# Performance work log

Measured on AMD Instinct MI355X. Metric: run time of the kernel, lower is better.

## Reference

```python
import jax, jax.numpy as jnp
import numpy as np

DIM = 1024
HEADS = 8
DIM_HEAD = 64
DIM_INNER = HEADS * DIM_HEAD  # 512


def setup_inputs() -> dict:
    key = jax.random.key(0)
    k1, k2, k3, k4 = jax.random.split(key, 4)
    x = jax.random.normal(k1, (1, 4096, DIM), dtype=jnp.float32)
    gamma = jnp.ones((DIM,), dtype=jnp.float32)
    w_qkv = jax.random.normal(k2, (DIM, 3 * DIM_INNER), dtype=jnp.float32) * (DIM ** -0.5)
    w_out = jax.random.normal(k3, (DIM_INNER, DIM), dtype=jnp.float32) * (DIM_INNER ** -0.5)
    return {"x": x, "gamma": gamma, "w_qkv": w_qkv, "w_out": w_out}


def _rmsnorm(x, gamma):
    # F.normalize(x, dim=-1) * sqrt(dim) * gamma
    norm = jnp.sqrt(jnp.sum(x * x, axis=-1, keepdims=True))
    x = x / jnp.maximum(norm, 1e-12)
    return x * (DIM ** 0.5) * gamma


def reference(x, gamma, w_qkv, w_out):
    b, n, _ = x.shape
    h, d = HEADS, DIM_HEAD
    normed = _rmsnorm(x, gamma)
    qkv = normed @ w_qkv  # [b, n, 3*h*d]
    qkv = qkv.reshape(b, n, 3, h, d)
    q = jnp.transpose(qkv[:, :, 0], (0, 2, 1, 3))  # b h n d
    k = jnp.transpose(qkv[:, :, 1], (0, 2, 1, 3))
    v = jnp.transpose(qkv[:, :, 2], (0, 2, 1, 3))
    # default_attention (faithful: scales q by d**0.5 as in source)
    q = q * (d ** 0.5)
    sim = jnp.einsum('bhid,bhjd->bhij', q, k)
    mask_value = -jnp.finfo(sim.dtype).max
    causal_mask = jnp.triu(jnp.ones((n, n), dtype=bool), 1)
    sim = jnp.where(causal_mask, mask_value, sim)
    attn = jax.nn.softmax(sim, axis=-1)
    out = jnp.einsum('bhij,bhjd->bhid', attn, v)  # b h n d
    out = jnp.transpose(out, (0, 2, 1, 3)).reshape(b, n, h * d)
    return out @ w_out  # [b, n, dim]
```

## Files before the change

### kernel.cpp

```cpp
#include <hip/hip_runtime.h>
#include <math.h>

#define SEQ 4096
#define DIM 1024
#define HEADS 8
#define DINNER 512
#define QKVW 1536
#define PAD 80
#define NCHUNK 4
#define CHUNK_KT 16

typedef unsigned short u16;
typedef __attribute__((ext_vector_type(8))) short s8v;
typedef __attribute__((ext_vector_type(4))) float f4v;
#define MFMA(a, b, c) __builtin_amdgcn_mfma_f32_16x16x32_bf16(a, b, c, 0, 0, 0)

__device__ __forceinline__ u16 f2bf(float f) {
    unsigned u = __float_as_uint(f);
    u += 0x7fff + ((u >> 16) & 1);
    return (u16)(u >> 16);
}
__device__ __forceinline__ float bf2f(u16 b) { return __uint_as_float(((unsigned)b) << 16); }

__global__ __launch_bounds__(256) void rmsnorm_split(const float* __restrict__ x,
                                                     const float* __restrict__ gamma,
                                                     u16* __restrict__ hi,
                                                     u16* __restrict__ lo) {
    __shared__ float red[4];
    const int row = blockIdx.x, t = threadIdx.x;
    const float* xr = x + (size_t)row * DIM;
    float v[4];
    float ss = 0.f;
#pragma unroll
    for (int i = 0; i < 4; ++i) { v[i] = xr[t + i * 256]; ss += v[i] * v[i]; }
#pragma unroll
    for (int off = 32; off >= 1; off >>= 1) ss += __shfl_xor(ss, off, 64);
    if ((t & 63) == 0) red[t >> 6] = ss;
    __syncthreads();
    float scale = 32.0f / fmaxf(sqrtf(red[0] + red[1] + red[2] + red[3]), 1e-12f);
#pragma unroll
    for (int i = 0; i < 4; ++i) {
        int c = t + i * 256;
        float y = v[i] * scale * gamma[c];
        u16 h = f2bf(y);
        hi[(size_t)row * DIM + c] = h;
        lo[(size_t)row * DIM + c] = f2bf(y - bf2f(h));
    }
}

__global__ __launch_bounds__(256) void transpose_split(const float* __restrict__ in,
                                                       u16* __restrict__ hi,
                                                       u16* __restrict__ lo,
                                                       int R, int C, int want_lo) {
    __shared__ float tile[64][65];
    const int c0 = blockIdx.x * 64, r0 = blockIdx.y * 64;
    const int t = threadIdx.x, col = t & 63, rb = t >> 6;
#pragma unroll
    for (int j = 0; j < 16; ++j)
        tile[rb + j * 4][col] = in[(size_t)(r0 + rb + j * 4) * C + c0 + col];
    __syncthreads();
#pragma unroll
    for (int j = 0; j < 16; ++j) {
        int cc = rb + j * 4;
        float v = tile[col][cc];
        size_t oi = (size_t)(c0 + cc) * R + r0 + col;
        u16 h = f2bf(v);
        hi[oi] = h;
        if (want_lo) lo[oi] = f2bf(v - bf2f(h));
    }
}

__global__ __launch_bounds__(256) void gemm_qkv_split(
    const u16* __restrict__ Ah, const u16* __restrict__ Al,
    const u16* __restrict__ Bh, const u16* __restrict__ Bl,
    u16* __restrict__ qh, u16* __restrict__ ql,
    u16* __restrict__ kh, u16* __restrict__ kl, u16* __restrict__ vtp) {
    __shared__ u16 Ash[64 * PAD], Asl[64 * PAD], Bsh[64 * PAD], Bsl[64 * PAD];
    const int t = threadIdx.x;
    const int bn = blockIdx.x * 64, bm = blockIdx.y * 64;
    const int w = t >> 6, lane = t & 63, m = lane & 15, q = lane >> 4;
    f4v acc[4] = {{0.f, 0.f, 0.f, 0.f}, {0.f, 0.f, 0.f, 0.f},
                  {0.f, 0.f, 0.f, 0.f}, {0.f, 0.f, 0.f, 0.f}};
    for (int k0 = 0; k0 < DIM; k0 += 64) {
        __syncthreads();
#pragma unroll
        for (int i = 0; i < 2; ++i) {
            int c = t + i * 256, row = c >> 3, ch = (c & 7) * 8;
            *(uint4*)&Ash[row * PAD + ch] = *(const uint4*)&Ah[(size_t)(bm + row) * DIM + k0 + ch];
            *(uint4*)&Asl[row * PAD + ch] = *(const uint4*)&Al[(size_t)(bm + row) * DIM + k0 + ch];
            *(uint4*)&Bsh[row * PAD + ch] = *(const uint4*)&Bh[(size_t)(bn + row) * DIM + k0 + ch];
            *(uint4*)&Bsl[row * PAD + ch] = *(const uint4*)&Bl[(size_t)(bn + row) * DIM + k0 + ch];
        }
        __syncthreads();
#pragma unroll
        for (int kk = 0; kk < 64; kk += 32) {
            s8v ah = *(const s8v*)&Ash[(w * 16 + m) * PAD + kk + q * 8];
            s8v al = *(const s8v*)&Asl[(w * 16 + m) * PAD + kk + q * 8];
#pragma unroll
            for (int ct = 0; ct < 4; ++ct) {
                s8v bh = *(const s8v*)&Bsh[(ct * 16 + m) * PAD + kk + q * 8];
                s8v bl = *(const s8v*)&Bsl[(ct * 16 + m) * PAD + kk + q * 8];
                acc[ct] = MFMA(ah, bh, acc[ct]);
                acc[ct] = MFMA(al, bh, acc[ct]);
                acc[ct] = MFMA(ah, bl, acc[ct]);
            }
        }
    }
    const int region = bn >> 9;
#pragma unroll
    for (int ct = 0; ct < 4; ++ct) {
#pragma unroll
        for (int r = 0; r < 4; ++r) {
            int gr = bm + w * 16 + q * 4 + r;
            int gc = bn + ct * 16 + m;
            float v = acc[ct][r];
            if (region == 0) {
                v *= 8.0f;
                u16 h = f2bf(v);
                qh[(size_t)gr * DINNER + gc] = h;
                ql[(size_t)gr * DINNER + gc] = f2bf(v - bf2f(h));
            } else if (region == 1) {
                u16 h = f2bf(v);
                kh[(size_t)gr * DINNER + (gc - 512)] = h;
                kl[(size_t)gr * DINNER + (gc - 512)] = f2bf(v - bf2f(h));
            } else {
                vtp[(size_t)(gc - 1024) * SEQ + gr] = f2bf(v);
            }
        }
    }
}

__global__ __launch_bounds__(256) void attn_part(
    const u16* __restrict__ qh, const u16* __restrict__ ql,
    const u16* __restrict__ kh, const u16* __restrict__ kl,
    const u16* __restrict__ vt, u16* __restrict__ po,
    float* __restrict__ pm, float* __restrict__ pl) {
    __shared__ u16 Qh[64 * PAD], Ql[64 * PAD], Kh[64 * PAD], Kl[64 * PAD],
                   Vt[64 * PAD], Ps[64 * PAD];
    const int qt = blockIdx.x, h = blockIdx.y, c = blockIdx.z;
    if (qt < c * CHUNK_KT) return;
    const int t = threadIdx.x;
    const int w = t >> 6, lane = t & 63, m = lane & 15, q = lane >> 4;
    const int kbeg = c * CHUNK_KT;
    const int kend = min(c * CHUNK_KT + CHUNK_KT, qt + 1);

#pragma unroll
    for (int i = 0; i < 2; ++i) {
        int cc = t + i * 256, row = cc >> 3, ch = (cc & 7) * 8;
        *(uint4*)&Qh[row * PAD + ch] =
            *(const uint4*)&qh[(size_t)(qt * 64 + row) * DINNER + h * 64 + ch];
        *(uint4*)&Ql[row * PAD + ch] =
            *(const uint4*)&ql[(size_t)(qt * 64 + row) * DINNER + h * 64 + ch];
    }

    f4v o[4] = {{0.f, 0.f, 0.f, 0.f}, {0.f, 0.f, 0.f, 0.f},
                {0.f, 0.f, 0.f, 0.f}, {0.f, 0.f, 0.f, 0.f}};
    float mi[4] = {-1e30f, -1e30f, -1e30f, -1e30f};
    float li[4] = {0.f, 0.f, 0.f, 0.f};

    uint4 rkh[2], rkl[2], rv[2];
    const int cc0 = t, cc1 = t + 256;
    const int prow0 = cc0 >> 3, pch0 = (cc0 & 7) * 8;
    const int prow1 = cc1 >> 3, pch1 = (cc1 & 7) * 8;

#define ISSUE(kt_)                                                                       \
    do {                                                                                 \
        rkh[0] = *(const uint4*)&kh[(size_t)((kt_)*64 + prow0) * DINNER + h * 64 + pch0];\
        rkh[1] = *(const uint4*)&kh[(size_t)((kt_)*64 + prow1) * DINNER + h * 64 + pch1];\
        rkl[0] = *(const uint4*)&kl[(size_t)((kt_)*64 + prow0) * DINNER + h * 64 + pch0];\
        rkl[1] = *(const uint4*)&kl[(size_t)((kt_)*64 + prow1) * DINNER + h * 64 + pch1];\
        rv[0]  = *(const uint4*)&vt[(size_t)(h * 64 + prow0) * SEQ + (kt_)*64 + pch0];   \
        rv[1]  = *(const uint4*)&vt[(size_t)(h * 64 + prow1) * SEQ + (kt_)*64 + pch1];   \
    } while (0)

    ISSUE(kbeg);

    for (int kt = kbeg; kt < kend; ++kt) {
        __syncthreads();
        *(uint4*)&Kh[prow0 * PAD + pch0] = rkh[0];
        *(uint4*)&Kh[prow1 * PAD + pch1] = rkh[1];
        *(uint4*)&Kl[prow0 * PAD + pch0] = rkl[0];
        *(uint4*)&Kl[prow1 * PAD + pch1] = rkl[1];
        *(uint4*)&Vt[prow0 * PAD + pch0] = rv[0];
        *(uint4*)&Vt[prow1 * PAD + pch1] = rv[1];
        __syncthreads();
        int ktn = (kt + 1 < kend) ? kt + 1 : kt;
        ISSUE(ktn);

        f4v s[4] = {{0.f, 0.f, 0.f, 0.f}, {0.f, 0.f, 0.f, 0.f},
                    {0.f, 0.f, 0.f, 0.f}, {0.f, 0.f, 0.f, 0.f}};
#pragma unroll
        for (int kk = 0; kk < 64; kk += 32) {
            s8v ah = *(const s8v*)&Qh[(w * 16 + m) * PAD + kk + q * 8];
            s8v al = *(const s8v*)&Ql[(w * 16 + m) * PAD + kk + q * 8];
#pragma unroll
            for (int ct = 0; ct < 4; ++ct) {
                s8v bh = *(const s8v*)&Kh[(ct * 16 + m) * PAD + kk + q * 8];
                s8v bl = *(const s8v*)&Kl[(ct * 16 + m) * PAD + kk + q * 8];
                s[ct] = MFMA(ah, bh, s[ct]);
                s[ct] = MFMA(al, bh, s[ct]);
                s[ct] = MFMA(ah, bl, s[ct]);
            }
        }
        if (kt == qt) {
#pragma unroll
            for (int ct = 0; ct < 4; ++ct)
#pragma unroll
                for (int r = 0; r < 4; ++r)
                    if (ct * 16 + m > w * 16 + q * 4 + r) s[ct][r] = -1e30f;
        }

        float alpha[4];
#pragma unroll
        for (int r = 0; r < 4; ++r) {
            float rm = fmaxf(fmaxf(s[0][r], s[1][r]), fmaxf(s[2][r], s[3][r]));
#pragma unroll
            for (int off = 8; off >= 1; off >>= 1) rm = fmaxf(rm, __shfl_xor(rm, off, 64));
            float mn = fmaxf(mi[r], rm);
            alpha[r] = __expf(mi[r] - mn);
            mi[r] = mn;
            float rs = 0.f;
#pragma unroll
            for (int ct = 0; ct < 4; ++ct) {
                s[ct][r] = __expf(s[ct][r] - mn);
                rs += s[ct][r];
            }
#pragma unroll
            for (int off = 8; off >= 1; off >>= 1) rs += __shfl_xor(rs, off, 64);
            li[r] = li[r] * alpha[r] + rs;
        }

#pragma unroll
        for (int ct = 0; ct < 4; ++ct)
#pragma unroll
            for (int r = 0; r < 4; ++r) {
                Ps[(w * 16 + q * 4 + r) * PAD + ct * 16 + m] = f2bf(s[ct][r]);
                o[ct][r] *= alpha[r];
            }
#pragma unroll
        for (int kk = 0; kk < 64; kk += 32) {
            s8v ap = *(const s8v*)&Ps[(w * 16 + m) * PAD + kk + q * 8];
#pragma unroll
            for (int ct = 0; ct < 4; ++ct) {
                s8v bv = *(const s8v*)&Vt[(ct * 16 + m) * PAD + kk + q * 8];
                o[ct] = MFMA(ap, bv, o[ct]);
            }
        }
    }
#undef ISSUE

#pragma unroll
    for (int r = 0; r < 4; ++r) {
        int grow = qt * 64 + w * 16 + q * 4 + r;
        size_t base = ((size_t)(c * HEADS + h) * SEQ + grow);
#pragma unroll
        for (int ct = 0; ct < 4; ++ct)
            po[base * 64 + ct * 16 + m] = f2bf(o[ct][r]);
        if (m == 0) { pm[base] = mi[r]; pl[base] = li[r]; }
    }
}

__global__ __launch_bounds__(256) void attn_merge(const u16* __restrict__ po,
                                                  const float* __restrict__ pm,
                                                  const float* __restrict__ pl,
                                                  u16* __restrict__ atto) {
    const int h = blockIdx.y;
    const int row = blockIdx.x * 4 + (threadIdx.x >> 6);
    const int d = threadIdx.x & 63;
    const int nc = (row >> 10) + 1;
    float M = -1e30f;
    for (int c = 0; c < nc; ++c)
        M = fmaxf(M, pm[(size_t)(c * HEADS + h) * SEQ + row]);
    float L = 0.f, O = 0.f;
    for (int c = 0; c < nc; ++c) {
        size_t base = (size_t)(c * HEADS + h) * SEQ + row;
        float e = __expf(pm[base] - M);
        L += pl[base] * e;
        O += bf2f(po[base * 64 + d]) * e;
    }
    atto[(size_t)row * DINNER + h * 64 + d] = f2bf(O / L);
}

__global__ __launch_bounds__(256) void gemm_out_bf16(const u16* __restrict__ A,
                                                     const u16* __restrict__ Bt,
                                                     float* __restrict__ C) {
    __shared__ u16 As[64 * PAD], Bs[64 * PAD];
    const int t = threadIdx.x;
    const int bn = blockIdx.x * 64, bm = blockIdx.y * 64;
    const int w = t >> 6, lane = t & 63, m = lane & 15, q = lane >> 4;
    f4v acc[4] = {{0.f, 0.f, 0.f, 0.f}, {0.f, 0.f, 0.f, 0.f},
                  {0.f, 0.f, 0.f, 0.f}, {0.f, 0.f, 0.f, 0.f}};
    for (int k0 = 0; k0 < DINNER; k0 += 64) {
        __syncthreads();
#pragma unroll
        for (int i = 0; i < 2; ++i) {
            int c = t + i * 256, row = c >> 3, ch = (c & 7) * 8;
            *(uint4*)&As[row * PAD + ch] = *(const uint4*)&A[(size_t)(bm + row) * DINNER + k0 + ch];
            *(uint4*)&Bs[row * PAD + ch] = *(const uint4*)&Bt[(size_t)(bn + row) * DINNER + k0 + ch];
        }
        __syncthreads();
#pragma unroll
        for (int kk = 0; kk < 64; kk += 32) {
            s8v a = *(const s8v*)&As[(w * 16 + m) * PAD + kk + q * 8];
#pragma unroll
            for (int ct = 0; ct < 4; ++ct) {
                s8v b = *(const s8v*)&Bs[(ct * 16 + m) * PAD + kk + q * 8];
                acc[ct] = MFMA(a, b, acc[ct]);
            }
        }
    }
#pragma unroll
    for (int ct = 0; ct < 4; ++ct)
#pragma unroll
        for (int r = 0; r < 4; ++r)
            C[(size_t)(bm + w * 16 + q * 4 + r) * DIM + bn + ct * 16 + m] = acc[ct][r];
}

extern "C" void kernel_launch(void* const* d_in, const int* in_sizes, int n_in,
                              void* d_out, int out_size, void* d_ws, size_t ws_size,
                              hipStream_t stream) {
    const float* x     = (const float*)d_in[0];
    const float* gamma = (const float*)d_in[1];
    const float* w_qkv = (const float*)d_in[2];
    const float* w_out = (const float*)d_in[3];
    float* out = (float*)d_out;

    u16* nh = (u16*)d_out;
    u16* nl = nh + (size_t)SEQ * DIM;
    u16* po = (u16*)d_out;

    u16* p = (u16*)d_ws;
    u16* wqt_h = p; p += (size_t)QKVW * DIM;
    u16* wqt_l = p; p += (size_t)QKVW * DIM;
    u16* wot   = p; p += (size_t)DIM * DINNER;
    u16* qh = p; p += (size_t)SEQ * DINNER;
    u16* ql = p; p += (size_t)SEQ * DINNER;
    u16* kh = p; p += (size_t)SEQ * DINNER;
    u16* kl = p; p += (size_t)SEQ * DINNER;
    u16* vt = p; p += (size_t)DINNER * SEQ;
    u16* atto = p; p += (size_t)SEQ * DINNER;
    float* pm = (float*)p; p += (size_t)2 * NCHUNK * HEADS * SEQ;
    float* pl = (float*)p; p += (size_t)2 * NCHUNK * HEADS * SEQ;

    transpose_split<<<dim3(QKVW / 64, DIM / 64), 256, 0, stream>>>(w_qkv, wqt_h, wqt_l,
                                                                   DIM, QKVW, 1);
    transpose_split<<<dim3(DIM / 64, DINNER / 64), 256, 0, stream>>>(w_out, wot, nullptr,
                                                                     DINNER, DIM, 0);
    rmsnorm_split<<<SEQ, 256, 0, stream>>>(x, gamma, nh, nl);
    gemm_qkv_split<<<dim3(QKVW / 64, SEQ / 64), 256, 0, stream>>>(nh, nl, wqt_h, wqt_l,
                                                                  qh, ql, kh, kl, vt);
    attn_part<<<dim3(SEQ / 64, HEADS, NCHUNK), 256, 0, stream>>>(qh, ql, kh, kl, vt,
                                                                 po, pm, pl);
    attn_merge<<<dim3(SEQ / 4, HEADS), 256, 0, stream>>>(po, pm, pl, atto);
    gemm_out_bf16<<<dim3(DIM / 64, SEQ / 64), 256, 0, stream>>>(atto, wot, out);
}
```

Baseline: 300.8 us.

## Load K/V/Q fragments directly from global into registers, halve KV chunks

The attention kernel stops staging Q, K and V tiles through shared memory with block-wide barriers. Each wave now loads its MFMA operand fragments straight from global memory into registers, and only the P tile goes through a per-wave LDS slice, so no __syncthreads is needed. Separately, the KV split goes from 4 chunks of 16 tiles to 2 chunks of 32 tiles, and the merge kernel is updated to match. The trade-off: each of the 4 waves re-reads the same K/V from global or cache with no software prefetch, giving up cross-wave reuse, and there is less split-K parallelism.

Measured after the change: 405.8 us. +34.9%, slower.

```diff
diff --git a/kernel.cpp b/kernel.cpp
--- a/kernel.cpp
+++ b/kernel.cpp
@@ -7,8 +7,9 @@
 #define DINNER 512
 #define QKVW 1536
 #define PAD 80
-#define NCHUNK 4
-#define CHUNK_KT 16
+#define PPAD 72
+#define NCHUNK 2
+#define CHUNK_KT 32
 
 typedef unsigned short u16;
 typedef __attribute__((ext_vector_type(8))) short s8v;
@@ -135,22 +136,21 @@
     const u16* __restrict__ kh, const u16* __restrict__ kl,
     const u16* __restrict__ vt, u16* __restrict__ po,
     float* __restrict__ pm, float* __restrict__ pl) {
-    __shared__ u16 Qh[64 * PAD], Ql[64 * PAD], Kh[64 * PAD], Kl[64 * PAD],
-                   Vt[64 * PAD], Ps[64 * PAD];
+    __shared__ u16 Ps[64 * PPAD];
     const int qt = blockIdx.x, h = blockIdx.y, c = blockIdx.z;
     if (qt < c * CHUNK_KT) return;
     const int t = threadIdx.x;
     const int w = t >> 6, lane = t & 63, m = lane & 15, q = lane >> 4;
     const int kbeg = c * CHUNK_KT;
-    const int kend = min(c * CHUNK_KT + CHUNK_KT, qt + 1);
-
-#pragma unroll
-    for (int i = 0; i < 2; ++i) {
-        int cc = t + i * 256, row = cc >> 3, ch = (cc & 7) * 8;
-        *(uint4*)&Qh[row * PAD + ch] =
-            *(const uint4*)&qh[(size_t)(qt * 64 + row) * DINNER + h * 64 + ch];
-        *(uint4*)&Ql[row * PAD + ch] =
-            *(const uint4*)&ql[(size_t)(qt * 64 + row) * DINNER + h * 64 + ch];
+    const int kend = min(kbeg + CHUNK_KT, qt + 1);
+    u16* myP = Ps + w * 16 * PPAD;
+
+    s8v qfh[2], qfl[2];
+#pragma unroll
+    for (int kkh = 0; kkh < 2; ++kkh) {
+        size_t a = (size_t)(qt * 64 + w * 16 + m) * DINNER + h * 64 + kkh * 32 + q * 8;
+        qfh[kkh] = *(const s8v*)&qh[a];
+        qfl[kkh] = *(const s8v*)&ql[a];
     }
 
     f4v o[4] = {{0.f, 0.f, 0.f, 0.f}, {0.f, 0.f, 0.f, 0.f},
@@ -158,50 +158,29 @@
     float mi[4] = {-1e30f, -1e30f, -1e30f, -1e30f};
     float li[4] = {0.f, 0.f, 0.f, 0.f};
 
-    uint4 rkh[2], rkl[2], rv[2];
-    const int cc0 = t, cc1 = t + 256;
-    const int prow0 = cc0 >> 3, pch0 = (cc0 & 7) * 8;
-    const int prow1 = cc1 >> 3, pch1 = (cc1 & 7) * 8;
-
-#define ISSUE(kt_)                                                                       \
-    do {                                                                                 \
-        rkh[0] = *(const uint4*)&kh[(size_t)((kt_)*64 + prow0) * DINNER + h * 64 + pch0];\
-        rkh[1] = *(const uint4*)&kh[(size_t)((kt_)*64 + prow1) * DINNER + h * 64 + pch1];\
-        rkl[0] = *(const uint4*)&kl[(size_t)((kt_)*64 + prow0) * DINNER + h * 64 + pch0];\
-        rkl[1] = *(const uint4*)&kl[(size_t)((kt_)*64 + prow1) * DINNER + h * 64 + pch1];\
-        rv[0]  = *(const uint4*)&vt[(size_t)(h * 64 + prow0) * SEQ + (kt_)*64 + pch0];   \
-        rv[1]  = *(const uint4*)&vt[(size_t)(h * 64 + prow1) * SEQ + (kt_)*64 + pch1];   \
-    } while (0)
-
-    ISSUE(kbeg);
-
     for (int kt = kbeg; kt < kend; ++kt) {
-        __syncthreads();
-        *(uint4*)&Kh[prow0 * PAD + pch0] = rkh[0];
-        *(uint4*)&Kh[prow1 * PAD + pch1] = rkh[1];
-        *(uint4*)&Kl[prow0 * PAD + pch0] = rkl[0];
-        *(uint4*)&Kl[prow1 * PAD + pch1] = rkl[1];
-        *(uint4*)&Vt[prow0 * PAD + pch0] = rv[0];
-        *(uint4*)&Vt[prow1 * PAD + pch1] = rv[1];
-        __syncthreads();
-        int ktn = (kt + 1 < kend) ? kt + 1 : kt;
-        ISSUE(ktn);
+        s8v kfh[2][4], kfl[2][4], vf[2][4];
+#pragma unroll
+        for (int kkh = 0; kkh < 2; ++kkh)
+#pragma unroll
+            for (int ct = 0; ct < 4; ++ct) {
+                size_t ka = (size_t)(kt * 64 + ct * 16 + m) * DINNER + h * 64 + kkh * 32 + q * 8;
+                kfh[kkh][ct] = *(const s8v*)&kh[ka];
+                kfl[kkh][ct] = *(const s8v*)&kl[ka];
+                vf[kkh][ct]  = *(const s8v*)&vt[(size_t)(h * 64 + ct * 16 + m) * SEQ +
+                                                kt * 64 + kkh * 32 + q * 8];
+            }
 
         f4v s[4] = {{0.f, 0.f, 0.f, 0.f}, {0.f, 0.f, 0.f, 0.f},
                     {0.f, 0.f, 0.f, 0.f}, {0.f, 0.f, 0.f, 0.f}};
 #pragma unroll
-        for (int kk = 0; kk < 64; kk += 32) {
-            s8v ah = *(const s8v*)&Qh[(w * 16 + m) * PAD + kk + q * 8];
-            s8v al = *(const s8v*)&Ql[(w * 16 + m) * PAD + kk + q * 8];
-#pragma unroll
-            for (int ct = 0; ct < 4; ++ct) {
-                s8v bh = *(const s8v*)&Kh[(ct * 16 + m) * PAD + kk + q * 8];
-                s8v bl = *(const s8v*)&Kl[(ct * 16 + m) * PAD + kk + q * 8];
-                s[ct] = MFMA(ah, bh, s[ct]);
-                s[ct] = MFMA(al, bh, s[ct]);
-                s[ct] = MFMA(ah, bl, s[ct]);
-            }
-        }
+        for (int kkh = 0; kkh < 2; ++kkh)
+#pragma unroll
+            for (int ct = 0; ct < 4; ++ct) {
+                s[ct] = MFMA(qfh[kkh], kfh[kkh][ct], s[ct]);
+                s[ct] = MFMA(qfl[kkh], kfh[kkh][ct], s[ct]);
+                s[ct] = MFMA(qfh[kkh], kfl[kkh][ct], s[ct]);
+            }
         if (kt == qt) {
 #pragma unroll
             for (int ct = 0; ct < 4; ++ct)
@@ -234,20 +213,17 @@
         for (int ct = 0; ct < 4; ++ct)
 #pragma unroll
             for (int r = 0; r < 4; ++r) {
-                Ps[(w * 16 + q * 4 + r) * PAD + ct * 16 + m] = f2bf(s[ct][r]);
+                myP[(q * 4 + r) * PPAD + ct * 16 + m] = f2bf(s[ct][r]);
                 o[ct][r] *= alpha[r];
             }
 #pragma unroll
-        for (int kk = 0; kk < 64; kk += 32) {
-            s8v ap = *(const s8v*)&Ps[(w * 16 + m) * PAD + kk + q * 8];
-#pragma unroll
-            for (int ct = 0; ct < 4; ++ct) {
-                s8v bv = *(const s8v*)&Vt[(ct * 16 + m) * PAD + kk + q * 8];
-                o[ct] = MFMA(ap, bv, o[ct]);
-            }
-        }
-    }
-#undef ISSUE
+        for (int kkh = 0; kkh < 2; ++kkh) {
+            s8v ap = *(const s8v*)&myP[m * PPAD + kkh * 32 + q * 8];
+#pragma unroll
+            for (int ct = 0; ct < 4; ++ct)
+                o[ct] = MFMA(ap, vf[kkh][ct], o[ct]);
+        }
+    }
 
 #pragma unroll
     for (int r = 0; r < 4; ++r) {
@@ -267,7 +243,7 @@
     const int h = blockIdx.y;
     const int row = blockIdx.x * 4 + (threadIdx.x >> 6);
     const int d = threadIdx.x & 63;
-    const int nc = (row >> 10) + 1;
+    const int nc = (row >> 11) + 1;
     float M = -1e30f;
     for (int c = 0; c < nc; ++c)
         M = fmaxf(M, pm[(size_t)(c * HEADS + h) * SEQ + row]);
```
